# Kernel optimization log

Hardware: AMD Instinct MI355X
Metric: run time of the kernel (lower is better)

## Reference

```python
import jax, jax.numpy as jnp
import numpy as np

B, T, C, H = 8, 1024, 1024, 16
HD = C // H  # head dim = 64
NEG = -1e9


def setup_inputs() -> dict:
    key = jax.random.key(0)
    ks = jax.random.split(key, 10)
    total = B * T
    x = jax.random.normal(ks[0], (total, C), dtype=jnp.float32)
    # identity pack: each padded row is a contiguous chunk of tokens
    padpack_index = jnp.arange(total, dtype=jnp.int64).reshape(B, T)
    # sorted per-row sequence ids -> block-diagonal attention within each packed row
    padpack_batch = jnp.sort(jax.random.randint(ks[1], (B, T), 0, 4, dtype=jnp.int32), axis=-1)
    padpack_inverse_index = jnp.arange(total, dtype=jnp.int64)
    s = 1.0 / np.sqrt(C)
    Wq = jax.random.uniform(ks[2], (C, C), jnp.float32, -s, s)
    bq = jax.random.uniform(ks[3], (C,), jnp.float32, -s, s)
    Wk = jax.random.uniform(ks[4], (C, C), jnp.float32, -s, s)
    bk = jax.random.uniform(ks[5], (C,), jnp.float32, -s, s)
    Wv = jax.random.uniform(ks[6], (C, C), jnp.float32, -s, s)
    bv = jax.random.uniform(ks[7], (C,), jnp.float32, -s, s)
    Wp = jax.random.uniform(ks[8], (C, C), jnp.float32, -s, s)
    bp = jax.random.uniform(ks[9], (C,), jnp.float32, -s, s)
    return {"x": x, "padpack_index": padpack_index, "padpack_batch": padpack_batch,
            "padpack_inverse_index": padpack_inverse_index,
            "Wq": Wq, "bq": bq, "Wk": Wk, "bk": bk, "Wv": Wv, "bv": bv, "Wp": Wp, "bp": bp}


def reference(x, padpack_index, padpack_batch, padpack_inverse_index,
              Wq, bq, Wk, bk, Wv, bv, Wp, bp):
    # gather ragged tokens into padded [B, T, C]
    xp = x[padpack_index]
    # torch Linear: y = x @ W.T + b
    q = (xp @ Wq.T + bq).reshape(B, T, H, HD)
    k = (xp @ Wk.T + bk).reshape(B, T, H, HD)
    v = (xp @ Wv.T + bv).reshape(B, T, H, HD)
    scale = 1.0 / np.sqrt(HD).astype(np.float32)
    att = jnp.einsum('bihd,bjhd->bhij', q, k) * scale  # [B,H,T,T]
    # mask: token pairs from different packed sequences cannot attend
    mask = (padpack_batch[:, :, None] != padpack_batch[:, None, :])[:, None]  # [B,1,T,T]
    att = jnp.where(mask, NEG, att)
    att = jax.nn.softmax(att, axis=-1)
    y = jnp.einsum('bhij,bjhd->bihd', att, v).reshape(B, T, C)
    y = y @ Wp.T + bp
    # scatter back to ragged layout [total_tokens, C]
    return y.reshape(B * T, C)[padpack_inverse_index]
```

## Files before the change

### kernel.cpp

```cpp
#include <hip/hip_runtime.h>


typedef __attribute__((ext_vector_type(8))) short short8;
typedef __attribute__((ext_vector_type(4))) float f32x4;

#define MFMA16(a, b, c) __builtin_amdgcn_mfma_f32_16x16x32_bf16((a), (b), (c), 0, 0, 0)

__device__ __forceinline__ ushort f2b(float f) {
  union { float f; unsigned u; } v; v.f = f;
  unsigned u = v.u;
  return (ushort)((u + 0x7fffu + ((u >> 16) & 1u)) >> 16);
}

__device__ __forceinline__ void gload16(const void* g, void* l) {
  __builtin_amdgcn_global_load_lds((const __attribute__((address_space(1))) unsigned int*)g,
                                   (__attribute__((address_space(3))) unsigned int*)l,
                                   16, 0, 0);
}

__device__ __forceinline__ void cvt4(const float* __restrict__ s, ushort* __restrict__ d) {
  const float4 v = *(const float4*)s;
  ushort4 r; r.x = f2b(v.x); r.y = f2b(v.y); r.z = f2b(v.z); r.w = f2b(v.w);
  *(ushort4*)d = r;
}

__global__ __launch_bounds__(256) void prep(const float* __restrict__ x,
    const float* __restrict__ wq, const float* __restrict__ wk,
    const float* __restrict__ wv, const float* __restrict__ wp,
    ushort* __restrict__ xb, ushort* __restrict__ wb,
    const int* __restrict__ pb, int* __restrict__ bnd) {
  const int bid = blockIdx.x;
  if (bid >= 12288) {
    const int b = bid - 12288;
    const int* p = pb + b * 1024;
    const int i = threadIdx.x;
#pragma unroll
    for (int e = 0; e < 4; ++e) {
      const int idx = i * 4 + e;
      const int cur = p[idx];
      const int prev = (idx == 0) ? -1 : p[idx - 1];
      for (int v = prev + 1; v <= cur; ++v) bnd[b * 8 + v] = idx;
    }
    if (i == 255) {
      const int cur = p[1023];
      for (int v = cur + 1; v <= 4; ++v) bnd[b * 8 + v] = 1024;
    }
    return;
  }
  const long long e0 = ((long long)bid * 256 + threadIdx.x) * 4;
  const long long NX = 8388608ll;
  if (e0 < NX) {
    cvt4(x + e0, xb + e0);
  } else {
    const long long t = e0 - NX;
    const int sel = (int)(t >> 20);
    const float* w = sel == 0 ? wq : sel == 1 ? wk : sel == 2 ? wv : wp;
    cvt4(w + (t & 1048575), wb + t);
  }
}

template <int MODE>
__global__ __launch_bounds__(512, 2) void gemm8(
    const ushort* __restrict__ A, const ushort* __restrict__ Bw,
    const float* __restrict__ bias0, const float* __restrict__ bias1,
    const float* __restrict__ bias2,
    ushort* __restrict__ O0, ushort* __restrict__ O1, ushort* __restrict__ O2,
    float* __restrict__ Of) {
  constexpr int ACH = 256 * 64;
  constexpr int BCH = 128 * 64;
  constexpr int BUFB = 2 * (ACH + BCH);
  __shared__ __align__(16) char smem[3 * BUFB];

  const int tid = threadIdx.x, lane = tid & 63, wid = tid >> 6;
  const int wr = wid >> 1, wc = wid & 1;
  const int lg = lane >> 4, lc = lane & 15;

  const int id = blockIdx.x;
  const int s = id >> 3;
  const int m0 = ((id & 7) * 4 + (s & 3)) << 8;
  const int n0 = (s >> 2) << 7;

  f32x4 acc[4][4] = {};

  const int sr0 = tid >> 2;
  const int sc0 = (tid & 3) ^ ((sr0 >> 1) & 3);

#define STAGE(dst_, kh, kt) { \
    char* ad = (dst_) + (kh) * ACH; \
    char* bd = (dst_) + 2 * ACH + (kh) * BCH; \
    const int kcol = (kt) * 64 + (kh) * 32; \
    gload16(A + (size_t)(m0 + sr0) * 1024 + kcol + sc0 * 8, ad + tid * 16); \
    gload16(A + (size_t)(m0 + 128 + sr0) * 1024 + kcol + sc0 * 8, ad + (tid + 512) * 16); \
    gload16(Bw + (size_t)(n0 + sr0) * 1024 + kcol + sc0 * 8, bd + tid * 16); \
  }

#define PHASE_COMPUTE(src_, kh) { \
    const char* ab = (src_) + (kh) * ACH; \
    const char* bb = (src_) + 2 * ACH + (kh) * BCH; \
    short8 af[4]; short8 bf[4]; \
    _Pragma("unroll") \
    for (int f = 0; f < 4; ++f) { \
      const int row = wr * 64 + f * 16 + lc; \
      af[f] = *(const short8*)(ab + row * 64 + ((lg ^ ((row >> 1) & 3)) << 4)); \
    } \
    _Pragma("unroll") \
    for (int g = 0; g < 4; ++g) { \
      const int row = wc * 64 + g * 16 + lc; \
      bf[g] = *(const short8*)(bb + row * 64 + ((lg ^ ((row >> 1) & 3)) << 4)); \
    } \
    asm volatile("s_waitcnt lgkmcnt(0)" ::: "memory"); \
    __builtin_amdgcn_sched_barrier(0); \
    __builtin_amdgcn_s_setprio(1); \
    _Pragma("unroll") \
    for (int f = 0; f < 4; ++f) \
      _Pragma("unroll") \
      for (int g = 0; g < 4; ++g) \
        acc[f][g] = MFMA16(af[f], bf[g], acc[f][g]); \
    __builtin_amdgcn_s_setprio(0); \
  }

#define WAITVM(n) { asm volatile("s_waitcnt vmcnt(" #n ")" ::: "memory"); }

  char* b0 = smem;
  char* b1 = smem + BUFB;
  char* b2 = smem + 2 * BUFB;

  STAGE(b0, 0, 0)
  STAGE(b0, 1, 0)
  STAGE(b1, 0, 1)
  STAGE(b1, 1, 1)

  for (int t = 0; t < 14; ++t) {
    WAITVM(9)
    __builtin_amdgcn_s_barrier();
    __builtin_amdgcn_sched_barrier(0);
    STAGE(b2, 0, t + 2)
    PHASE_COMPUTE(b0, 0)
    WAITVM(9)
    __builtin_amdgcn_s_barrier();
    __builtin_amdgcn_sched_barrier(0);
    STAGE(b2, 1, t + 2)
    PHASE_COMPUTE(b0, 1)
    char* tmp = b0; b0 = b1; b1 = b2; b2 = tmp;
  }
  WAITVM(9)
  __builtin_amdgcn_s_barrier();
  __builtin_amdgcn_sched_barrier(0);
  PHASE_COMPUTE(b0, 0)
  WAITVM(6)
  __builtin_amdgcn_s_barrier();
  __builtin_amdgcn_sched_barrier(0);
  PHASE_COMPUTE(b0, 1)
  WAITVM(3)
  __builtin_amdgcn_s_barrier();
  __builtin_amdgcn_sched_barrier(0);
  PHASE_COMPUTE(b1, 0)
  WAITVM(0)
  __builtin_amdgcn_s_barrier();
  __builtin_amdgcn_sched_barrier(0);
  PHASE_COMPUTE(b1, 1)

  if constexpr (MODE == 0) {
    const int sel = n0 >> 10, nloc = n0 & 1023;
    const float* bias = sel == 0 ? bias0 : sel == 1 ? bias1 : bias2;
    float bval[4];
#pragma unroll
    for (int g = 0; g < 4; ++g) bval[g] = bias[nloc + wc * 64 + g * 16 + lc];
    if (sel < 2) {
      ushort* dst = sel ? O1 : O0;
#pragma unroll
      for (int f = 0; f < 4; ++f)
#pragma unroll
        for (int j = 0; j < 4; ++j) {
          const size_t row = m0 + wr * 64 + f * 16 + lg * 4 + j;
#pragma unroll
          for (int g = 0; g < 4; ++g)
            dst[row * 1024 + nloc + wc * 64 + g * 16 + lc] = f2b(acc[f][g][j] + bval[g]);
        }
    } else {
      ushort (*Ts)[136] = (ushort(*)[136])smem;
#pragma unroll
      for (int mh = 0; mh < 2; ++mh) {
        __syncthreads();
        if ((wr >> 1) == mh) {
#pragma unroll
          for (int f = 0; f < 4; ++f)
#pragma unroll
            for (int g = 0; g < 4; ++g)
#pragma unroll
              for (int j = 0; j < 4; ++j)
                Ts[(wr & 1) * 64 + f * 16 + lg * 4 + j][wc * 64 + g * 16 + lc] =
                    f2b(acc[f][g][j] + bval[g]);
        }
        __syncthreads();
        const int c = tid >> 2;
        const int th = (tid & 3) * 32;
        const int gt = m0 + mh * 128;
        const int b = gt >> 10;
        const int t0 = (gt & 1023) + th;
        const int gc = nloc + c;
        ushort* dp = O2 + ((size_t)((b * 16 + (gc >> 6)) * 64 + (gc & 63))) * 1024 + t0;
#pragma unroll
        for (int gb = 0; gb < 4; ++gb) {
          short8 pk;
#pragma unroll
          for (int u = 0; u < 8; ++u) pk[u] = (short)Ts[th + gb * 8 + u][c];
          *(short8*)(dp + gb * 8) = pk;
        }
      }
    }
  } else {
    float bval[4];
#pragma unroll
    for (int g = 0; g < 4; ++g) bval[g] = bias0[n0 + wc * 64 + g * 16 + lc];
#pragma unroll
    for (int f = 0; f < 4; ++f)
#pragma unroll
      for (int j = 0; j < 4; ++j) {
        const size_t row = m0 + wr * 64 + f * 16 + lg * 4 + j;
#pragma unroll
        for (int g = 0; g < 4; ++g)
          Of[row * 1024 + n0 + wc * 64 + g * 16 + lc] = acc[f][g][j] + bval[g];
      }
  }
#undef STAGE
#undef PHASE_COMPUTE
#undef WAITVM
}

__global__ __launch_bounds__(512) void attn(const ushort* __restrict__ Q,
    const ushort* __restrict__ K, const ushort* __restrict__ Vt,
    const int* __restrict__ bnd, ushort* __restrict__ O) {
  __shared__ __align__(16) char kvbuf[2][16384];
  __shared__ __align__(16) ushort Plds[8][16][68];

  const int tid = threadIdx.x, lane = tid & 63, w = tid >> 6;
  const int lg = lane >> 4, lc = lane & 15;

  const int id = blockIdx.x;
  const int xcd = id & 7, slot = id >> 3;
  const int bh = xcd + 8 * (slot >> 3);
  const int qt = slot & 7;
  const int b = bh >> 4, h = bh & 15;
  const int q0 = qt * 128 + w * 16;

  const int* bd = bnd + b * 8;
  const int b1 = bd[1], b2 = bd[2], b3 = bd[3], b4 = bd[4];
#define SEGID(k) (((k) >= b1) + ((k) >= b2) + ((k) >= b3) + ((k) >= b4))

  const int qid = SEGID(q0 + lc);
  int klo_l = (qid > 0) ? b1 : 0;
  klo_l = (qid > 1) ? b2 : klo_l;
  klo_l = (qid > 2) ? b3 : klo_l;
  int khi_l = (qid > 0) ? b2 : b1;
  khi_l = (qid > 1) ? b3 : khi_l;
  khi_l = (qid > 2) ? b4 : khi_l;

  const int bq_lo = SEGID(qt * 128), bq_hi = SEGID(qt * 128 + 127);
  unsigned am = 0;
#pragma unroll
  for (int jt = 0; jt < 16; ++jt) {
    const int tlo = SEGID(jt * 64), thi = SEGID(jt * 64 + 63);
    if (thi >= bq_lo && tlo <= bq_hi) am |= (1u << jt);
  }

  const ushort* qp = Q + (size_t)(b * 1024 + q0 + lc) * 1024 + h * 64 + lg * 8;
  const short8 qf0 = *(const short8*)qp;
  const short8 qf1 = *(const short8*)(qp + 32);

  const int r0 = tid >> 3;
  const int c16 = (tid & 7) ^ (r0 & 7);
  const ushort* Kg = K + (size_t)(b * 1024 + r0) * 1024 + h * 64 + c16 * 8;
  const ushort* Vg = Vt + (size_t)(bh * 64 + r0) * 1024 + c16 * 8;

#define STAGE(bufp, j) { \
    gload16(Kg + (size_t)(j) * 1024, (bufp) + tid * 16); \
    gload16(Vg + (j), (bufp) + 8192 + tid * 16); }

#define SOFF(r, ch) ((r) * 128 + ((((ch) ^ ((r) & 7))) << 4))

  float mr = -1e30f, lr = 0.f;
  f32x4 o[4] = {};

  unsigned rem = am;
  int jc = __builtin_ctz(rem) * 64;
  rem &= rem - 1;
  STAGE(kvbuf[0], jc)
  __syncthreads();
  int cur = 0;

  for (;;) {
    int jn = -1;
    if (rem) {
      jn = __builtin_ctz(rem) * 64;
      rem &= rem - 1;
      STAGE(kvbuf[cur ^ 1], jn)
    }
    const char* bufK = kvbuf[cur];
    const char* bufV = kvbuf[cur] + 8192;

    short8 kf[8];
#pragma unroll
    for (int n = 0; n < 4; ++n) {
      const int rr = n * 16 + lc;
      kf[2 * n] = *(const short8*)(bufK + SOFF(rr, lg));
      kf[2 * n + 1] = *(const short8*)(bufK + SOFF(rr, lg + 4));
    }
    f32x4 s[4];
    __builtin_amdgcn_s_setprio(1);
#pragma unroll
    for (int n = 0; n < 4; ++n) {
      f32x4 z = {};
      z = MFMA16(kf[2 * n], qf0, z);
      s[n] = MFMA16(kf[2 * n + 1], qf1, z);
    }
    __builtin_amdgcn_s_setprio(0);

#pragma unroll
    for (int n = 0; n < 4; ++n) {
      const int kk = jc + n * 16 + lg * 4;
#pragma unroll
      for (int r = 0; r < 4; ++r) {
        const bool ok = (kk + r >= klo_l) && (kk + r < khi_l);
        s[n][r] = ok ? s[n][r] * 0.125f : -1e9f;
      }
    }

    float rm = fmaxf(fmaxf(fmaxf(s[0][0], s[0][1]), fmaxf(s[0][2], s[0][3])),
                     fmaxf(fmaxf(fmaxf(s[1][0], s[1][1]), fmaxf(s[1][2], s[1][3])),
                           fmaxf(fmaxf(fmaxf(s[2][0], s[2][1]), fmaxf(s[2][2], s[2][3])),
                                 fmaxf(fmaxf(s[3][0], s[3][1]), fmaxf(s[3][2], s[3][3])))));
    rm = fmaxf(rm, __shfl_xor(rm, 16));
    rm = fmaxf(rm, __shfl_xor(rm, 32));
    float mn = mr;
    if (!__all(rm <= mr + 8.f)) {
      mn = fmaxf(mr, rm);
      const float sf = __expf(mr - mn);
      mr = mn;
      lr *= sf;
      const float s0 = __shfl(sf, lg * 4 + 0);
      const float s1 = __shfl(sf, lg * 4 + 1);
      const float s2 = __shfl(sf, lg * 4 + 2);
      const float s3 = __shfl(sf, lg * 4 + 3);
#pragma unroll
      for (int n = 0; n < 4; ++n) {
        o[n][0] *= s0; o[n][1] *= s1; o[n][2] *= s2; o[n][3] *= s3;
      }
    }
    float rs = 0.f;
#pragma unroll
    for (int n = 0; n < 4; ++n)
#pragma unroll
      for (int r = 0; r < 4; ++r) {
        const float p = __expf(s[n][r] - mn);
        s[n][r] = p; rs += p;
      }
    rs += __shfl_xor(rs, 16);
    rs += __shfl_xor(rs, 32);
    lr += rs;

#pragma unroll
    for (int n = 0; n < 4; ++n) {
      ushort4 pk;
      pk.x = f2b(s[n][0]); pk.y = f2b(s[n][1]); pk.z = f2b(s[n][2]); pk.w = f2b(s[n][3]);
      *(ushort4*)&Plds[w][lc][n * 16 + lg * 4] = pk;
    }
    asm volatile("s_waitcnt lgkmcnt(0)" ::: "memory");
    __builtin_amdgcn_sched_barrier(0);
    const short8 p0 = *(const short8*)&Plds[w][lc][lg * 8];
    const short8 p1 = *(const short8*)&Plds[w][lc][32 + lg * 8];
    __builtin_amdgcn_sched_barrier(0);

    short8 vv[8];
#pragma unroll
    for (int n = 0; n < 4; ++n) {
      const int rr = n * 16 + lc;
      vv[2 * n] = *(const short8*)(bufV + SOFF(rr, lg));
      vv[2 * n + 1] = *(const short8*)(bufV + SOFF(rr, lg + 4));
    }
    __builtin_amdgcn_s_setprio(1);
#pragma unroll
    for (int n = 0; n < 4; ++n) {
      o[n] = MFMA16(p0, vv[2 * n], o[n]);
      o[n] = MFMA16(p1, vv[2 * n + 1], o[n]);
    }
    __builtin_amdgcn_s_setprio(0);

    if (jn < 0) break;
    __syncthreads();
    cur ^= 1;
    jc = jn;
  }

  const float linv = 1.f / lr;
  const float i0 = __shfl(linv, lg * 4 + 0);
  const float i1 = __shfl(linv, lg * 4 + 1);
  const float i2 = __shfl(linv, lg * 4 + 2);
  const float i3 = __shfl(linv, lg * 4 + 3);
#pragma unroll
  for (int n = 0; n < 4; ++n) {
    const size_t base = (size_t)(b * 1024 + q0) * 1024 + h * 64 + n * 16 + lc;
    O[base + 0 * 1024 + (size_t)lg * 4096] = f2b(o[n][0] * i0);
    O[base + 1 * 1024 + (size_t)lg * 4096] = f2b(o[n][1] * i1);
    O[base + 2 * 1024 + (size_t)lg * 4096] = f2b(o[n][2] * i2);
    O[base + 3 * 1024 + (size_t)lg * 4096] = f2b(o[n][3] * i3);
  }
#undef STAGE
#undef SOFF
#undef SEGID
}

extern "C" void kernel_launch(void* const* d_in, const int* in_sizes, int n_in,
                              void* d_out, int out_size, void* d_ws, size_t ws_size,
                              hipStream_t stream) {
  const float* x  = (const float*)d_in[0];
  const int*  pb  = (const int*)d_in[2];
  const float* Wq = (const float*)d_in[4]; const float* bq = (const float*)d_in[5];
  const float* Wk = (const float*)d_in[6]; const float* bk = (const float*)d_in[7];
  const float* Wv = (const float*)d_in[8]; const float* bv = (const float*)d_in[9];
  const float* Wp = (const float*)d_in[10]; const float* bp = (const float*)d_in[11];
  float* out = (float*)d_out;
  char* ws = (char*)d_ws;

  ushort* xb = (ushort*)ws;
  ushort* wb = (ushort*)(ws + (16u << 20));
  ushort* Qb = (ushort*)(ws + (24u << 20));
  ushort* Kb = (ushort*)(ws + (40u << 20));
  ushort* Vt = (ushort*)(ws + (56u << 20));
  int*    bnd = (int*)(ws + (72u << 20));
  ushort* Ob = xb;

  prep<<<12296, 256, 0, stream>>>(x, Wq, Wk, Wv, Wp, xb, wb, pb, bnd);
  gemm8<0><<<768, 512, 0, stream>>>(xb, wb, bq, bk, bv, Qb, Kb, Vt, nullptr);
  attn<<<1024, 512, 0, stream>>>(Qb, Kb, Vt, bnd, Ob);
  gemm8<1><<<256, 512, 0, stream>>>(Ob, wb + (3 << 20), bp,
                                    nullptr, nullptr, nullptr, nullptr, nullptr, out);
}
```

Baseline: 149.0 us.

## Transpose attention P through ds_bpermute instead of LDS, relax GEMM barriers

The attention kernel no longer writes P to a per-wave LDS scratch and reads it back. It packs probabilities with v_cvt_pk_bf16_f32 and rearranges them across lanes with ds_bpermute into the MFMA A-operand layout, which removes the LDS buffer and an explicit lgkmcnt wait. The GEMM also drops its explicit lgkmcnt(0) wait and sched_barrier after the fragment loads, and replaces the sched_barrier after each s_barrier with a compiler memory clobber, giving the scheduler more freedom to interleave work. The risk is a wrong lane mapping, and the compiler may insert waits that are less well placed.

```diff
diff --git a/kernel.cpp b/kernel.cpp
--- a/kernel.cpp
+++ b/kernel.cpp
@@ -3,6 +3,7 @@
 
 typedef __attribute__((ext_vector_type(8))) short short8;
 typedef __attribute__((ext_vector_type(4))) float f32x4;
+typedef __attribute__((ext_vector_type(4))) unsigned uint4v;
 
 #define MFMA16(a, b, c) __builtin_amdgcn_mfma_f32_16x16x32_bf16((a), (b), (c), 0, 0, 0)
 
@@ -108,8 +109,6 @@
       const int row = wc * 64 + g * 16 + lc; \
       bf[g] = *(const short8*)(bb + row * 64 + ((lg ^ ((row >> 1) & 3)) << 4)); \
     } \
-    asm volatile("s_waitcnt lgkmcnt(0)" ::: "memory"); \
-    __builtin_amdgcn_sched_barrier(0); \
     __builtin_amdgcn_s_setprio(1); \
     _Pragma("unroll") \
     for (int f = 0; f < 4; ++f) \
@@ -120,6 +119,7 @@
   }
 
 #define WAITVM(n) { asm volatile("s_waitcnt vmcnt(" #n ")" ::: "memory"); }
+#define BARF() { __builtin_amdgcn_s_barrier(); asm volatile("" ::: "memory"); }
 
   char* b0 = smem;
   char* b1 = smem + BUFB;
@@ -132,32 +132,26 @@
 
   for (int t = 0; t < 14; ++t) {
     WAITVM(9)
-    __builtin_amdgcn_s_barrier();
-    __builtin_amdgcn_sched_barrier(0);
+    BARF()
     STAGE(b2, 0, t + 2)
     PHASE_COMPUTE(b0, 0)
     WAITVM(9)
-    __builtin_amdgcn_s_barrier();
-    __builtin_amdgcn_sched_barrier(0);
+    BARF()
     STAGE(b2, 1, t + 2)
     PHASE_COMPUTE(b0, 1)
     char* tmp = b0; b0 = b1; b1 = b2; b2 = tmp;
   }
   WAITVM(9)
-  __builtin_amdgcn_s_barrier();
-  __builtin_amdgcn_sched_barrier(0);
+  BARF()
   PHASE_COMPUTE(b0, 0)
   WAITVM(6)
-  __builtin_amdgcn_s_barrier();
-  __builtin_amdgcn_sched_barrier(0);
+  BARF()
   PHASE_COMPUTE(b0, 1)
   WAITVM(3)
-  __builtin_amdgcn_s_barrier();
-  __builtin_amdgcn_sched_barrier(0);
+  BARF()
   PHASE_COMPUTE(b1, 0)
   WAITVM(0)
-  __builtin_amdgcn_s_barrier();
-  __builtin_amdgcn_sched_barrier(0);
+  BARF()
   PHASE_COMPUTE(b1, 1)
 
   if constexpr (MODE == 0) {
@@ -226,15 +220,15 @@
 #undef STAGE
 #undef PHASE_COMPUTE
 #undef WAITVM
+#undef BARF
 }
 
 __global__ __launch_bounds__(512) void attn(const ushort* __restrict__ Q,
     const ushort* __restrict__ K, const ushort* __restrict__ Vt,
     const int* __restrict__ bnd, ushort* __restrict__ O) {
   __shared__ __align__(16) char kvbuf[2][16384];
-  __shared__ __align__(16) ushort Plds[8][16][68];
-
-  const int tid = threadIdx.x, lane = tid & 63, w = tid >> 6;
+
+  const int tid = threadIdx.x, lane = tid & 63;
   const int lg = lane >> 4, lc = lane & 15;
 
   const int id = blockIdx.x;
@@ -242,7 +236,7 @@
   const int bh = xcd + 8 * (slot >> 3);
   const int qt = slot & 7;
   const int b = bh >> 4, h = bh & 15;
-  const int q0 = qt * 128 + w * 16;
+  const int q0 = qt * 128 + (tid >> 6) * 16;
 
   const int* bd = bnd + b * 8;
   const int b1 = bd[1], b2 = bd[2], b3 = bd[3], b4 = bd[4];
@@ -288,6 +282,10 @@
   STAGE(kvbuf[0], jc)
   __syncthreads();
   int cur = 0;
+
+  const int aA = ((lane & 16) << 3) + ((lane & 15) << 2);
+  const int aB = aA + 64;
+  const bool hi = (lane & 32) != 0;
 
   for (;;) {
     int jn = -1;
@@ -359,17 +357,32 @@
     rs += __shfl_xor(rs, 32);
     lr += rs;
 
-#pragma unroll
-    for (int n = 0; n < 4; ++n) {
-      ushort4 pk;
-      pk.x = f2b(s[n][0]); pk.y = f2b(s[n][1]); pk.z = f2b(s[n][2]); pk.w = f2b(s[n][3]);
-      *(ushort4*)&Plds[w][lc][n * 16 + lg * 4] = pk;
-    }
-    asm volatile("s_waitcnt lgkmcnt(0)" ::: "memory");
-    __builtin_amdgcn_sched_barrier(0);
-    const short8 p0 = *(const short8*)&Plds[w][lc][lg * 8];
-    const short8 p1 = *(const short8*)&Plds[w][lc][32 + lg * 8];
-    __builtin_amdgcn_sched_barrier(0);
+    unsigned u[4][2];
+#pragma unroll
+    for (int n = 0; n < 4; ++n) {
+      asm("v_cvt_pk_bf16_f32 %0, %1, %2" : "=v"(u[n][0]) : "v"(s[n][0]), "v"(s[n][1]));
+      asm("v_cvt_pk_bf16_f32 %0, %1, %2" : "=v"(u[n][1]) : "v"(s[n][2]), "v"(s[n][3]));
+    }
+    uint4v pwm[2];
+#pragma unroll
+    for (int m = 0; m < 2; ++m) {
+      const unsigned x0 = __builtin_amdgcn_ds_bpermute(aA, u[2 * m][0]);
+      const unsigned y0 = __builtin_amdgcn_ds_bpermute(aA, u[2 * m + 1][0]);
+      const unsigned x1 = __builtin_amdgcn_ds_bpermute(aA, u[2 * m][1]);
+      const unsigned y1 = __builtin_amdgcn_ds_bpermute(aA, u[2 * m + 1][1]);
+      const unsigned x2 = __builtin_amdgcn_ds_bpermute(aB, u[2 * m][0]);
+      const unsigned y2 = __builtin_amdgcn_ds_bpermute(aB, u[2 * m + 1][0]);
+      const unsigned x3 = __builtin_amdgcn_ds_bpermute(aB, u[2 * m][1]);
+      const unsigned y3 = __builtin_amdgcn_ds_bpermute(aB, u[2 * m + 1][1]);
+      uint4v w;
+      w.x = hi ? y0 : x0;
+      w.y = hi ? y1 : x1;
+      w.z = hi ? y2 : x2;
+      w.w = hi ? y3 : x3;
+      pwm[m] = w;
+    }
+    const short8 p0 = *reinterpret_cast<const short8*>(&pwm[0]);
+    const short8 p1 = *reinterpret_cast<const short8*>(&pwm[1]);
 
     short8 vv[8];
 #pragma unroll
```

After: 149.9 us. Within noise of the previous version (+0.6%).
